# Kernel optimization log

Measured on AMD Instinct MI355X. Metric: run time of the kernel, lower is better.

Reference implementation:

```python
import jax, jax.numpy as jnp
import numpy as np

G = 128            # fine grid side -> N0 = 16384 nodes
C = 128            # hidden channels
CL = 4             # voxel cluster side (scale = CL/G = 1/32)
GC = G // CL       # coarse grid side = 32
NC = GC * GC       # 1024 coarse nodes
L = 6              # 3 MP blocks (down0, down1, up0) x 2 MP layers each


def _build_graph():
    ii, jj = np.meshgrid(np.arange(G), np.arange(G), indexing='ij')
    nid = ii * G + jj
    s_h, t_h = nid[:, :-1].ravel(), nid[:, 1:].ravel()
    s_v, t_v = nid[:-1, :].ravel(), nid[1:, :].ravel()
    src = np.concatenate([s_h, t_h, s_v, t_v]).astype(np.int64)
    dst = np.concatenate([t_h, s_h, t_v, s_v]).astype(np.int64)
    # voxel_grid(pos, size=1/32) on the unit square -> cluster id per node
    perm = ((ii // CL) * GC + (jj // CL)).ravel().astype(np.int64)
    ms, mt = perm[src], perm[dst]
    key = ms * NC + mt
    nonself = ms != mt
    uk = np.unique(key[nonself])                  # pool_edge: remove self loops + coalesce (sorted)
    E1 = int(uk.shape[0])
    e2c = np.where(nonself, np.searchsorted(uk, key), E1).astype(np.int64)
    pooled_ei = np.stack([uk // NC, uk % NC]).astype(np.int64)
    # unpool_edge: first fine edge whose mapped endpoints match each coarse edge
    first = np.full(E1 + 1, src.shape[0], dtype=np.int64)
    np.minimum.at(first, e2c, np.arange(src.shape[0], dtype=np.int64))
    perm_edges = first[:E1]
    return np.stack([src, dst]), perm, pooled_ei, e2c, perm_edges


def setup_inputs() -> dict:
    key = jax.random.key(0)
    ks = jax.random.split(key, 10)
    ei, perm, pei, e2c, pe = _build_graph()
    N0, E0 = G * G, ei.shape[1]
    s = 0.05
    return {
        'x': jax.random.normal(ks[0], (N0, C), jnp.float32),
        'edge_attr': jax.random.normal(ks[1], (E0, C), jnp.float32),
        'We1': jax.random.normal(ks[2], (L, 3 * C, C), jnp.float32) * s,
        'be1': jax.random.normal(ks[3], (L, C), jnp.float32) * s,
        'We2': jax.random.normal(ks[4], (L, C, C), jnp.float32) * s,
        'be2': jax.random.normal(ks[5], (L, C), jnp.float32) * s,
        'Wn1': jax.random.normal(ks[6], (L, 2 * C, C), jnp.float32) * s,
        'bn1': jax.random.normal(ks[7], (L, C), jnp.float32) * s,
        'Wn2': jax.random.normal(ks[8], (L, C, C), jnp.float32) * s,
        'bn2': jax.random.normal(ks[9], (L, C), jnp.float32) * s,
        'edge_index': jnp.asarray(ei),
        'perm': jnp.asarray(perm),
        'pooled_edge_index': jnp.asarray(pei),
        'edge_to_coarse': jnp.asarray(e2c),
        'perm_edges': jnp.asarray(pe),
    }


def _mp_block(x, e, src, dst, n, layers, We1, be1, We2, be2, Wn1, bn1, Wn2, bn2):
    # Residual message-passing block: edge MLP on [e, x_src, x_dst], node MLP on [x, sum_msg]
    for l in layers:
        m = jnp.concatenate([e, x[src], x[dst]], axis=-1)          # [E, 3C]
        e = e + (jax.nn.relu(m @ We1[l] + be1[l]) @ We2[l] + be2[l])
        agg = jax.ops.segment_sum(e, dst, num_segments=n)          # [N, C]
        h = jnp.concatenate([x, agg], axis=-1)                     # [N, 2C]
        x = x + (jax.nn.relu(h @ Wn1[l] + bn1[l]) @ Wn2[l] + bn2[l])
    return x, e


def reference(x, edge_attr, We1, be1, We2, be2, Wn1, bn1, Wn2, bn2,
              edge_index, perm, pooled_edge_index, edge_to_coarse, perm_edges):
    p = (We1, be1, We2, be2, Wn1, bn1, Wn2, bn2)
    N0 = x.shape[0]
    src0, dst0 = edge_index[0], edge_index[1]
    # down conv 0 (fine level)
    x0, e0 = _mp_block(x, edge_attr, src0, dst0, N0, (0, 1), *p)
    # avg_pool: mean node features per cluster, coalesce-sum edge attrs
    counts = jax.ops.segment_sum(jnp.ones((N0, 1), x.dtype), perm, num_segments=NC)
    x1 = jax.ops.segment_sum(x0, perm, num_segments=NC) / counts
    E1 = pooled_edge_index.shape[1]
    ea1 = jax.ops.segment_sum(e0, edge_to_coarse, num_segments=E1 + 1)[:E1]
    # down conv 1 (coarse level)
    x1, ea1 = _mp_block(x1, ea1, pooled_edge_index[0], pooled_edge_index[1], NC, (2, 3), *p)
    # unpool + sum-res skip connections
    xu = x0 + x1[perm]
    eu = e0 + jnp.zeros_like(e0).at[perm_edges].set(ea1)
    # up conv
    return _mp_block(xu, eu, src0, dst0, N0, (4, 5), *p)
```

## Files before the change

kernel.cpp:

```cpp
#include <hip/hip_runtime.h>

#define C_ 128
#define N0 16384
#define E0 65024
#define NC_ 1024
#define E1C 3968
#define LSTR 40

typedef __attribute__((ext_vector_type(8))) short bf16x8;
typedef __attribute__((ext_vector_type(4))) float f32x4;

#define OFF_WE1 0
#define OFF_WE2 294912
#define OFF_WN1 393216
#define OFF_WN2 589824
#define W_TOTAL 688128

__device__ __forceinline__ void bsplit(float a, unsigned short& hi, unsigned short& lo) {
  unsigned ab = __float_as_uint(a);
  unsigned hb = ab & 0xFFFF0000u;
  hi = (unsigned short)(hb >> 16);
  float r = a - __uint_as_float(hb);
  lo = (unsigned short)(__float_as_uint(r) >> 16);
}

__device__ __forceinline__ int cprefix(int ci, int cj) {
  int rows = (ci == 0) ? 0 : (94 + (ci - 1) * 126);
  int v = (ci > 0) + (ci < 31);
  int within = (cj == 0) ? 0 : (2 * cj - 1);
  return rows + within + cj * v;
}

__device__ __forceinline__ void add4(float4& s, const float* p) {
  float4 v = *(const float4*)p;
  s.x += v.x; s.y += v.y; s.z += v.z; s.w += v.w;
}

__global__ void prep_weights(const float* __restrict__ We1, const float* __restrict__ We2,
                             const float* __restrict__ Wn1, const float* __restrict__ Wn2,
                             short* __restrict__ wh, short* __restrict__ wl) {
  int idx = blockIdx.x * 256 + threadIdx.x;
  const float* src; int Kt, off, rem;
  if (idx < 294912)      { src = We1; Kt = 384; off = OFF_WE1; rem = idx; }
  else if (idx < 393216) { src = We2; Kt = 128; off = OFF_WE2; rem = idx - 294912; }
  else if (idx < 589824) { src = Wn1; Kt = 256; off = OFF_WN1; rem = idx - 393216; }
  else                   { src = Wn2; Kt = 128; off = OFF_WN2; rem = idx - 589824; }
  int per_layer = Kt << 7;
  int layer = rem / per_layer;
  int r2 = rem - layer * per_layer;
  int k = r2 >> 7;
  int col = r2 & 127;
  float a = src[layer * per_layer + (k << 7) + col];
  unsigned short hi, lo;
  bsplit(a, hi, lo);
  int dst = off + layer * ((Kt >> 5) << 12) + ((k >> 5) << 12) + (col << 5) + (k & 31);
  wh[dst] = (short)hi;
  wl[dst] = (short)lo;
}

template<int MODE>
__global__ __launch_bounds__(256, 2) void mlp_mfma(
    float* __restrict__ io, const float* __restrict__ xin,
    const int* __restrict__ srcI, const int* __restrict__ dstI,
    const short* __restrict__ W1h, const short* __restrict__ W1l,
    const float* __restrict__ b1,
    const short* __restrict__ W2h, const short* __restrict__ W2l,
    const float* __restrict__ b2)
{
  __shared__ alignas(16) short sAh[64 * LSTR], sAl[64 * LSTR];
  __shared__ alignas(16) short sWh[128 * LSTR], sWl[128 * LSTR];
  __shared__ int sS[64], sD[64];

  const int tid = threadIdx.x;
  const int r0 = blockIdx.x * 64;
  const int w   = tid >> 6;
  const int l   = tid & 63;
  const int c15 = l & 15;
  const int kg  = l >> 4;

  if (MODE == 0) {
    if (tid < 64) sS[tid] = srcI[r0 + tid];
    else if (tid < 128) sD[tid - 64] = dstI[r0 + tid - 64];
    __syncthreads();
  }

  f32x4 acc[8];
  #pragma unroll
  for (int t = 0; t < 8; ++t) acc[t] = (f32x4){0.f, 0.f, 0.f, 0.f};

  const int NKT = (MODE == 0) ? 12 : 8;
  for (int kt = 0; kt < NKT; ++kt) {
    const int region = kt >> 2;
    const int colbase = (kt & 3) * 32;
    #pragma unroll
    for (int tt = 0; tt < 2; ++tt) {
      int s = tid * 2 + tt;
      int row = s >> 3, q = s & 7;
      const float* rp;
      if (MODE == 0) {
        rp = (region == 0) ? io + (r0 + row) * C_
           : (region == 1) ? xin + sS[row] * C_
                           : xin + sD[row] * C_;
      } else {
        rp = (region == 0) ? io + (r0 + row) * C_ : xin + (r0 + row) * C_;
      }
      float4 a = *(const float4*)(rp + colbase + q * 4);
      unsigned short h0,h1,h2,h3, q0,q1,q2,q3;
      bsplit(a.x, h0, q0); bsplit(a.y, h1, q1);
      bsplit(a.z, h2, q2); bsplit(a.w, h3, q3);
      *(uint2*)&sAh[row * LSTR + q * 4] =
          make_uint2((unsigned)h0 | ((unsigned)h1 << 16), (unsigned)h2 | ((unsigned)h3 << 16));
      *(uint2*)&sAl[row * LSTR + q * 4] =
          make_uint2((unsigned)q0 | ((unsigned)q1 << 16), (unsigned)q2 | ((unsigned)q3 << 16));
    }
    {
      const short* srcH = W1h + (kt << 12);
      const short* srcL = W1l + (kt << 12);
      #pragma unroll
      for (int u0 = 0; u0 < 2; ++u0) {
        int u = tid + u0 * 256;
        int col = u >> 2, part = u & 3;
        *(uint4*)&sWh[col * LSTR + part * 8] = *(const uint4*)(srcH + u * 8);
        *(uint4*)&sWl[col * LSTR + part * 8] = *(const uint4*)(srcL + u * 8);
      }
    }
    __syncthreads();
    bf16x8 ah = *(const bf16x8*)&sAh[(w * 16 + c15) * LSTR + kg * 8];
    bf16x8 al = *(const bf16x8*)&sAl[(w * 16 + c15) * LSTR + kg * 8];
    #pragma unroll
    for (int t = 0; t < 8; ++t) {
      bf16x8 wh = *(const bf16x8*)&sWh[(t * 16 + c15) * LSTR + kg * 8];
      bf16x8 wl = *(const bf16x8*)&sWl[(t * 16 + c15) * LSTR + kg * 8];
      acc[t] = __builtin_amdgcn_mfma_f32_16x16x32_bf16(ah, wh, acc[t], 0, 0, 0);
      acc[t] = __builtin_amdgcn_mfma_f32_16x16x32_bf16(ah, wl, acc[t], 0, 0, 0);
      acc[t] = __builtin_amdgcn_mfma_f32_16x16x32_bf16(al, wh, acc[t], 0, 0, 0);
    }
    __syncthreads();
  }

  float b1v[8];
  #pragma unroll
  for (int t = 0; t < 8; ++t) b1v[t] = b1[t * 16 + c15];

  f32x4 acc2[8];
  #pragma unroll
  for (int t = 0; t < 8; ++t) acc2[t] = (f32x4){0.f, 0.f, 0.f, 0.f};

  #pragma unroll
  for (int kc = 0; kc < 4; ++kc) {
    __syncthreads();
    #pragma unroll
    for (int tt = 0; tt < 2; ++tt) {
      const int t = kc * 2 + tt;
      #pragma unroll
      for (int r = 0; r < 4; ++r) {
        float h = fmaxf(acc[t][r] + b1v[t], 0.f);
        unsigned short hh, hl;
        bsplit(h, hh, hl);
        int row = w * 16 + kg * 4 + r;
        int k = tt * 16 + c15;
        sAh[row * LSTR + k] = (short)hh;
        sAl[row * LSTR + k] = (short)hl;
      }
    }
    {
      const short* srcH = W2h + (kc << 12);
      const short* srcL = W2l + (kc << 12);
      #pragma unroll
      for (int u0 = 0; u0 < 2; ++u0) {
        int u = tid + u0 * 256;
        int col = u >> 2, part = u & 3;
        *(uint4*)&sWh[col * LSTR + part * 8] = *(const uint4*)(srcH + u * 8);
        *(uint4*)&sWl[col * LSTR + part * 8] = *(const uint4*)(srcL + u * 8);
      }
    }
    __syncthreads();
    bf16x8 ah = *(const bf16x8*)&sAh[(w * 16 + c15) * LSTR + kg * 8];
    bf16x8 al = *(const bf16x8*)&sAl[(w * 16 + c15) * LSTR + kg * 8];
    #pragma unroll
    for (int t = 0; t < 8; ++t) {
      bf16x8 wh = *(const bf16x8*)&sWh[(t * 16 + c15) * LSTR + kg * 8];
      bf16x8 wl = *(const bf16x8*)&sWl[(t * 16 + c15) * LSTR + kg * 8];
      acc2[t] = __builtin_amdgcn_mfma_f32_16x16x32_bf16(ah, wh, acc2[t], 0, 0, 0);
      acc2[t] = __builtin_amdgcn_mfma_f32_16x16x32_bf16(ah, wl, acc2[t], 0, 0, 0);
      acc2[t] = __builtin_amdgcn_mfma_f32_16x16x32_bf16(al, wh, acc2[t], 0, 0, 0);
    }
  }

  #pragma unroll
  for (int t = 0; t < 8; ++t) {
    float b2v = b2[t * 16 + c15];
    #pragma unroll
    for (int r = 0; r < 4; ++r) {
      int row = r0 + w * 16 + kg * 4 + r;
      float* p = io + row * C_ + t * 16 + c15;
      *p += acc2[t][r] + b2v;
    }
  }
}

__global__ void agg_fine(const float* __restrict__ e, float* __restrict__ agg) {
  int idx = blockIdx.x * 256 + threadIdx.x;
  int n = idx >> 5;
  int c4 = (idx & 31) * 4;
  int i = n >> 7, j = n & 127;
  float4 s = make_float4(0.f, 0.f, 0.f, 0.f);
  if (j >= 1)   add4(s, e + (i*127 + (j-1)) * C_ + c4);
  if (j <= 126) add4(s, e + (16256 + i*127 + j) * C_ + c4);
  if (i >= 1)   add4(s, e + (32512 + (i-1)*128 + j) * C_ + c4);
  if (i <= 126) add4(s, e + (48768 + i*128 + j) * C_ + c4);
  *(float4*)(agg + n * C_ + c4) = s;
}

__global__ void agg_coarse(const float* __restrict__ e1, float* __restrict__ agg1) {
  int idx = blockIdx.x * 256 + threadIdx.x;
  int m = idx >> 5;
  int c4 = (idx & 31) * 4;
  int ci = m >> 5, cj = m & 31;
  float4 s = make_float4(0.f, 0.f, 0.f, 0.f);
  if (ci > 0)  add4(s, e1 + (cprefix(ci-1,cj) + (ci-1>0) + (cj>0) + (cj<31)) * C_ + c4);
  if (cj > 0)  add4(s, e1 + (cprefix(ci,cj-1) + (ci>0) + (cj-1>0)) * C_ + c4);
  if (cj < 31) add4(s, e1 + (cprefix(ci,cj+1) + (ci>0)) * C_ + c4);
  if (ci < 31) add4(s, e1 + (cprefix(ci+1,cj)) * C_ + c4);
  *(float4*)(agg1 + m * C_ + c4) = s;
}

__global__ void pool_x(const float* __restrict__ x, float* __restrict__ x1) {
  int idx = blockIdx.x * 256 + threadIdx.x;
  int m = idx >> 5;
  int c4 = (idx & 31) * 4;
  int ci = m >> 5, cj = m & 31;
  float4 s = make_float4(0.f, 0.f, 0.f, 0.f);
  #pragma unroll
  for (int a = 0; a < 4; ++a)
    #pragma unroll
    for (int b = 0; b < 4; ++b)
      add4(s, x + ((4*ci + a) * 128 + 4*cj + b) * C_ + c4);
  s.x *= 0.0625f; s.y *= 0.0625f; s.z *= 0.0625f; s.w *= 0.0625f;
  *(float4*)(x1 + m * C_ + c4) = s;
}

__global__ void pool_e(const float* __restrict__ e, float* __restrict__ e1) {
  int idx = blockIdx.x * 256 + threadIdx.x;
  int combo = idx >> 5;
  int c4 = (idx & 31) * 4;
  int m = combo >> 2, dir = combo & 3;
  int ci = m >> 5, cj = m & 31;
  int cid, f0, fstep;
  if (dir == 0) { if (ci == 0) return;
    cid = cprefix(ci,cj);
    f0 = 48768 + (4*ci - 1) * 128 + 4*cj; fstep = 1;
  } else if (dir == 1) { if (cj == 0) return;
    cid = cprefix(ci,cj) + (ci>0);
    f0 = 16256 + (4*ci) * 127 + 4*cj - 1; fstep = 127;
  } else if (dir == 2) { if (cj == 31) return;
    cid = cprefix(ci,cj) + (ci>0) + (cj>0);
    f0 = (4*ci) * 127 + 4*cj + 3; fstep = 127;
  } else { if (ci == 31) return;
    cid = cprefix(ci,cj) + (ci>0) + (cj>0) + (cj<31);
    f0 = 32512 + (4*ci + 3) * 128 + 4*cj; fstep = 1;
  }
  float4 s = make_float4(0.f, 0.f, 0.f, 0.f);
  #pragma unroll
  for (int k = 0; k < 4; ++k)
    add4(s, e + (f0 + k * fstep) * C_ + c4);
  *(float4*)(e1 + cid * C_ + c4) = s;
}

__global__ void unpool_x(float* __restrict__ x, const float* __restrict__ x1,
                         const int* __restrict__ perm) {
  int idx = blockIdx.x * 256 + threadIdx.x;
  int n = idx >> 5, c4 = (idx & 31) * 4;
  int m = perm[n];
  float4 v = *(const float4*)(x + n * C_ + c4);
  add4(v, x1 + m * C_ + c4);
  *(float4*)(x + n * C_ + c4) = v;
}

__global__ void unpool_e(float* __restrict__ e, const float* __restrict__ e1,
                         const int* __restrict__ pe) {
  int idx = blockIdx.x * 256 + threadIdx.x;
  int k = idx >> 5, c4 = (idx & 31) * 4;
  int fe = pe[k];
  float4 v = *(const float4*)(e + fe * C_ + c4);
  add4(v, e1 + k * C_ + c4);
  *(float4*)(e + fe * C_ + c4) = v;
}

extern "C" void kernel_launch(void* const* d_in, const int* in_sizes, int n_in,
                              void* d_out, int out_size, void* d_ws, size_t ws_size,
                              hipStream_t stream) {
  const float* in_x  = (const float*)d_in[0];
  const float* in_ea = (const float*)d_in[1];
  const float* We1 = (const float*)d_in[2];
  const float* be1 = (const float*)d_in[3];
  const float* We2 = (const float*)d_in[4];
  const float* be2 = (const float*)d_in[5];
  const float* Wn1 = (const float*)d_in[6];
  const float* bn1 = (const float*)d_in[7];
  const float* Wn2 = (const float*)d_in[8];
  const float* bn2 = (const float*)d_in[9];
  const int* ei   = (const int*)d_in[10];
  const int* perm = (const int*)d_in[11];
  const int* pei  = (const int*)d_in[12];
  const int* pe   = (const int*)d_in[14];

  float* x = (float*)d_out;
  float* e = x + (size_t)N0 * C_;
  float* agg  = (float*)d_ws;
  float* x1   = agg + (size_t)N0 * C_;
  float* e1   = x1 + (size_t)NC_ * C_;
  float* agg1 = e1 + (size_t)E1C * C_;
  short* wsH  = (short*)(agg1 + (size_t)NC_ * C_);
  short* wsL  = wsH + W_TOTAL;

  hipMemcpyAsync(x, in_x, (size_t)N0 * C_ * 4, hipMemcpyDeviceToDevice, stream);
  hipMemcpyAsync(e, in_ea, (size_t)E0 * C_ * 4, hipMemcpyDeviceToDevice, stream);

  prep_weights<<<W_TOTAL / 256, 256, 0, stream>>>(We1, We2, Wn1, Wn2, wsH, wsL);

  const int* srcF = ei;  const int* dstF = ei + E0;
  const int* srcC = pei; const int* dstC = pei + E1C;

  #define WE1_OFF(l) (OFF_WE1 + (l) * 49152)
  #define WE2_OFF(l) (OFF_WE2 + (l) * 16384)
  #define WN1_OFF(l) (OFF_WN1 + (l) * 32768)
  #define WN2_OFF(l) (OFF_WN2 + (l) * 16384)

  for (int l = 0; l < 2; ++l) {
    mlp_mfma<0><<<E0/64, 256, 0, stream>>>(e, x, srcF, dstF,
        wsH + WE1_OFF(l), wsL + WE1_OFF(l), be1 + l*C_,
        wsH + WE2_OFF(l), wsL + WE2_OFF(l), be2 + l*C_);
    agg_fine<<<N0*32/256, 256, 0, stream>>>(e, agg);
    mlp_mfma<1><<<N0/64, 256, 0, stream>>>(x, agg, nullptr, nullptr,
        wsH + WN1_OFF(l), wsL + WN1_OFF(l), bn1 + l*C_,
        wsH + WN2_OFF(l), wsL + WN2_OFF(l), bn2 + l*C_);
  }

  pool_x<<<NC_*32/256, 256, 0, stream>>>(x, x1);
  pool_e<<<NC_*4*32/256, 256, 0, stream>>>(e, e1);

  for (int l = 2; l < 4; ++l) {
    mlp_mfma<0><<<E1C/64, 256, 0, stream>>>(e1, x1, srcC, dstC,
        wsH + WE1_OFF(l), wsL + WE1_OFF(l), be1 + l*C_,
        wsH + WE2_OFF(l), wsL + WE2_OFF(l), be2 + l*C_);
    agg_coarse<<<NC_*32/256, 256, 0, stream>>>(e1, agg1);
    mlp_mfma<1><<<NC_/64, 256, 0, stream>>>(x1, agg1, nullptr, nullptr,
        wsH + WN1_OFF(l), wsL + WN1_OFF(l), bn1 + l*C_,
        wsH + WN2_OFF(l), wsL + WN2_OFF(l), bn2 + l*C_);
  }

  unpool_x<<<N0*32/256, 256, 0, stream>>>(x, x1, perm);
  unpool_e<<<E1C*32/256, 256, 0, stream>>>(e, e1, pe);

  for (int l = 4; l < 6; ++l) {
    mlp_mfma<0><<<E0/64, 256, 0, stream>>>(e, x, srcF, dstF,
        wsH + WE1_OFF(l), wsL + WE1_OFF(l), be1 + l*C_,
        wsH + WE2_OFF(l), wsL + WE2_OFF(l), be2 + l*C_);
    agg_fine<<<N0*32/256, 256, 0, stream>>>(e, agg);
    mlp_mfma<1><<<N0/64, 256, 0, stream>>>(x, agg, nullptr, nullptr,
        wsH + WN1_OFF(l), wsL + WN1_OFF(l), bn1 + l*C_,
        wsH + WN2_OFF(l), wsL + WN2_OFF(l), bn2 + l*C_);
  }
}
```

Before: 475.3 us.

## Retile MLP kernel to 128-row blocks with 32x32 MFMA and register-prefetched A

Each block of the fused two-layer MLP kernel now covers 128 rows instead of 64. Its four waves are arranged 2x2, and each wave computes a 64x64 output tile with 32x32x16 bf16 MFMAs. A-operand rows are loaded straight from global memory into registers, split into hi/lo bf16 there, and the next k-chunk is prefetched before the barrier. The old LDS A staging buffer is gone, and the hidden activation is stored as packed hi/lo in a single LDS buffer. The aim is to halve weight staging per row, raise MFMA efficiency and cut LDS traffic, at the cost of higher register pressure and far fewer blocks (only 128 for node MLPs and 8 at the coarse level), which may leave many CUs idle.

```diff
diff --git a/kernel.cpp b/kernel.cpp
--- a/kernel.cpp
+++ b/kernel.cpp
@@ -6,9 +6,10 @@
 #define NC_ 1024
 #define E1C 3968
 #define LSTR 40
+#define HSTR 36
 
 typedef __attribute__((ext_vector_type(8))) short bf16x8;
-typedef __attribute__((ext_vector_type(4))) float f32x4;
+typedef __attribute__((ext_vector_type(16))) float f32x16;
 
 #define OFF_WE1 0
 #define OFF_WE2 294912
@@ -34,6 +35,13 @@
 __device__ __forceinline__ void add4(float4& s, const float* p) {
   float4 v = *(const float4*)p;
   s.x += v.x; s.y += v.y; s.z += v.z; s.w += v.w;
+}
+
+__device__ __forceinline__ f32x16 zero16() {
+  f32x16 z;
+  #pragma unroll
+  for (int i = 0; i < 16; ++i) z[i] = 0.f;
+  return z;
 }
 
 __global__ void prep_weights(const float* __restrict__ We1, const float* __restrict__ We2,
@@ -58,6 +66,44 @@
   wl[dst] = (short)lo;
 }
 
+__device__ __forceinline__ void stage_w(short* sWh, short* sWl,
+                                        const short* __restrict__ Wh,
+                                        const short* __restrict__ Wl,
+                                        int kc, int tid) {
+  const short* srcH = Wh + (kc << 12);
+  const short* srcL = Wl + (kc << 12);
+  #pragma unroll
+  for (int u0 = 0; u0 < 2; ++u0) {
+    int u = tid + u0 * 256;
+    int col = u >> 2, part = u & 3;
+    *(uint4*)&sWh[col * LSTR + part * 8] = *(const uint4*)(srcH + u * 8);
+    *(uint4*)&sWl[col * LSTR + part * 8] = *(const uint4*)(srcL + u * 8);
+  }
+}
+
+#define BSPLIT8(V0, V1, AH, AL) do { \
+    unsigned short h0_,h1_,h2_,h3_,h4_,h5_,h6_,h7_, l0_,l1_,l2_,l3_,l4_,l5_,l6_,l7_; \
+    bsplit((V0).x,h0_,l0_); bsplit((V0).y,h1_,l1_); bsplit((V0).z,h2_,l2_); bsplit((V0).w,h3_,l3_); \
+    bsplit((V1).x,h4_,l4_); bsplit((V1).y,h5_,l5_); bsplit((V1).z,h6_,l6_); bsplit((V1).w,h7_,l7_); \
+    AH = (bf16x8){(short)h0_,(short)h1_,(short)h2_,(short)h3_,(short)h4_,(short)h5_,(short)h6_,(short)h7_}; \
+    AL = (bf16x8){(short)l0_,(short)l1_,(short)l2_,(short)l3_,(short)l4_,(short)l5_,(short)l6_,(short)l7_}; \
+  } while (0)
+
+#define MFMA3(ACC, AH, AL, BH, BL) do { \
+    ACC = __builtin_amdgcn_mfma_f32_32x32x16_bf16(AH, BH, ACC, 0, 0, 0); \
+    ACC = __builtin_amdgcn_mfma_f32_32x32x16_bf16(AH, BL, ACC, 0, 0, 0); \
+    ACC = __builtin_amdgcn_mfma_f32_32x32x16_bf16(AL, BH, ACC, 0, 0, 0); \
+  } while (0)
+
+#define UNPACKH(ROW, S, AH, AL) do { \
+    const unsigned* hp_ = &sH[(ROW) * HSTR + (S) * 16 + hi * 8]; \
+    uint4 u0_ = *(const uint4*)hp_; uint4 u1_ = *(const uint4*)(hp_ + 4); \
+    AH = (bf16x8){(short)(u0_.x & 0xFFFFu), (short)(u0_.y & 0xFFFFu), (short)(u0_.z & 0xFFFFu), (short)(u0_.w & 0xFFFFu), \
+                  (short)(u1_.x & 0xFFFFu), (short)(u1_.y & 0xFFFFu), (short)(u1_.z & 0xFFFFu), (short)(u1_.w & 0xFFFFu)}; \
+    AL = (bf16x8){(short)(u0_.x >> 16), (short)(u0_.y >> 16), (short)(u0_.z >> 16), (short)(u0_.w >> 16), \
+                  (short)(u1_.x >> 16), (short)(u1_.y >> 16), (short)(u1_.z >> 16), (short)(u1_.w >> 16)}; \
+  } while (0)
+
 template<int MODE>
 __global__ __launch_bounds__(256, 2) void mlp_mfma(
     float* __restrict__ io, const float* __restrict__ xin,
@@ -67,136 +113,133 @@
     const short* __restrict__ W2h, const short* __restrict__ W2l,
     const float* __restrict__ b2)
 {
-  __shared__ alignas(16) short sAh[64 * LSTR], sAl[64 * LSTR];
   __shared__ alignas(16) short sWh[128 * LSTR], sWl[128 * LSTR];
-  __shared__ int sS[64], sD[64];
+  __shared__ alignas(16) unsigned sH[128 * HSTR];
 
   const int tid = threadIdx.x;
-  const int r0 = blockIdx.x * 64;
   const int w   = tid >> 6;
+  const int wr  = w >> 1;
+  const int wc  = w & 1;
   const int l   = tid & 63;
-  const int c15 = l & 15;
-  const int kg  = l >> 4;
-
+  const int c31 = l & 31;
+  const int hi  = l >> 5;
+  const int r0  = blockIdx.x * 128;
+
+  const int ar0 = wr * 64 + c31;
+  const int ar1 = ar0 + 32;
+  const float* pio0 = io + (size_t)(r0 + ar0) * C_;
+  const float* pio1 = io + (size_t)(r0 + ar1) * C_;
+  const float *px0, *px1, *pd0, *pd1;
   if (MODE == 0) {
-    if (tid < 64) sS[tid] = srcI[r0 + tid];
-    else if (tid < 128) sD[tid - 64] = dstI[r0 + tid - 64];
+    px0 = xin + (size_t)srcI[r0 + ar0] * C_;
+    px1 = xin + (size_t)srcI[r0 + ar1] * C_;
+    pd0 = xin + (size_t)dstI[r0 + ar0] * C_;
+    pd1 = xin + (size_t)dstI[r0 + ar1] * C_;
+  } else {
+    px0 = xin + (size_t)(r0 + ar0) * C_;
+    px1 = xin + (size_t)(r0 + ar1) * C_;
+    pd0 = px0; pd1 = px1;
+  }
+
+  float4 pa00, pa01, pa02, pa03, pa10, pa11, pa12, pa13;
+#define LOADA(KC) do { \
+    int rg_ = (KC) >> 2; int cb_ = ((KC) & 3) * 32 + hi * 8; \
+    const float* q0_; const float* q1_; \
+    if (MODE == 0) { q0_ = (rg_ == 0) ? pio0 : (rg_ == 1) ? px0 : pd0; \
+                     q1_ = (rg_ == 0) ? pio1 : (rg_ == 1) ? px1 : pd1; } \
+    else           { q0_ = (rg_ == 0) ? pio0 : px0; \
+                     q1_ = (rg_ == 0) ? pio1 : px1; } \
+    pa00 = *(const float4*)(q0_ + cb_);      pa01 = *(const float4*)(q0_ + cb_ + 4); \
+    pa02 = *(const float4*)(q0_ + cb_ + 16); pa03 = *(const float4*)(q0_ + cb_ + 20); \
+    pa10 = *(const float4*)(q1_ + cb_);      pa11 = *(const float4*)(q1_ + cb_ + 4); \
+    pa12 = *(const float4*)(q1_ + cb_ + 16); pa13 = *(const float4*)(q1_ + cb_ + 20); \
+  } while (0)
+
+  f32x16 acc00 = zero16(), acc01 = zero16(), acc10 = zero16(), acc11 = zero16();
+
+  const int NK1 = (MODE == 0) ? 12 : 8;
+  LOADA(0);
+  for (int kc = 0; kc < NK1; ++kc) {
+    bf16x8 ah0s0, al0s0, ah0s1, al0s1, ah1s0, al1s0, ah1s1, al1s1;
+    BSPLIT8(pa00, pa01, ah0s0, al0s0);
+    BSPLIT8(pa02, pa03, ah0s1, al0s1);
+    BSPLIT8(pa10, pa11, ah1s0, al1s0);
+    BSPLIT8(pa12, pa13, ah1s1, al1s1);
+    if (kc + 1 < NK1) LOADA(kc + 1);
     __syncthreads();
-  }
-
-  f32x4 acc[8];
-  #pragma unroll
-  for (int t = 0; t < 8; ++t) acc[t] = (f32x4){0.f, 0.f, 0.f, 0.f};
-
-  const int NKT = (MODE == 0) ? 12 : 8;
-  for (int kt = 0; kt < NKT; ++kt) {
-    const int region = kt >> 2;
-    const int colbase = (kt & 3) * 32;
+    stage_w(sWh, sWl, W1h, W1l, kc, tid);
+    __syncthreads();
     #pragma unroll
-    for (int tt = 0; tt < 2; ++tt) {
-      int s = tid * 2 + tt;
-      int row = s >> 3, q = s & 7;
-      const float* rp;
-      if (MODE == 0) {
-        rp = (region == 0) ? io + (r0 + row) * C_
-           : (region == 1) ? xin + sS[row] * C_
-                           : xin + sD[row] * C_;
+    for (int s = 0; s < 2; ++s) {
+      const int wb = s * 16 + hi * 8;
+      bf16x8 bh0 = *(const bf16x8*)&sWh[(wc * 64 + c31) * LSTR + wb];
+      bf16x8 bl0 = *(const bf16x8*)&sWl[(wc * 64 + c31) * LSTR + wb];
+      bf16x8 bh1 = *(const bf16x8*)&sWh[(wc * 64 + 32 + c31) * LSTR + wb];
+      bf16x8 bl1 = *(const bf16x8*)&sWl[(wc * 64 + 32 + c31) * LSTR + wb];
+      if (s == 0) {
+        MFMA3(acc00, ah0s0, al0s0, bh0, bl0);
+        MFMA3(acc01, ah0s0, al0s0, bh1, bl1);
+        MFMA3(acc10, ah1s0, al1s0, bh0, bl0);
+        MFMA3(acc11, ah1s0, al1s0, bh1, bl1);
       } else {
-        rp = (region == 0) ? io + (r0 + row) * C_ : xin + (r0 + row) * C_;
-      }
-      float4 a = *(const float4*)(rp + colbase + q * 4);
-      unsigned short h0,h1,h2,h3, q0,q1,q2,q3;
-      bsplit(a.x, h0, q0); bsplit(a.y, h1, q1);
-      bsplit(a.z, h2, q2); bsplit(a.w, h3, q3);
-      *(uint2*)&sAh[row * LSTR + q * 4] =
-          make_uint2((unsigned)h0 | ((unsigned)h1 << 16), (unsigned)h2 | ((unsigned)h3 << 16));
-      *(uint2*)&sAl[row * LSTR + q * 4] =
-          make_uint2((unsigned)q0 | ((unsigned)q1 << 16), (unsigned)q2 | ((unsigned)q3 << 16));
-    }
-    {
-      const short* srcH = W1h + (kt << 12);
-      const short* srcL = W1l + (kt << 12);
-      #pragma unroll
-      for (int u0 = 0; u0 < 2; ++u0) {
-        int u = tid + u0 * 256;
-        int col = u >> 2, part = u & 3;
-        *(uint4*)&sWh[col * LSTR + part * 8] = *(const uint4*)(srcH + u * 8);
-        *(uint4*)&sWl[col * LSTR + part * 8] = *(const uint4*)(srcL + u * 8);
+        MFMA3(acc00, ah0s1, al0s1, bh0, bl0);
+        MFMA3(acc01, ah0s1, al0s1, bh1, bl1);
+        MFMA3(acc10, ah1s1, al1s1, bh0, bl0);
+        MFMA3(acc11, ah1s1, al1s1, bh1, bl1);
       }
     }
-    __syncthreads();
-    bf16x8 ah = *(const bf16x8*)&sAh[(w * 16 + c15) * LSTR + kg * 8];
-    bf16x8 al = *(const bf16x8*)&sAl[(w * 16 + c15) * LSTR + kg * 8];
-    #pragma unroll
-    for (int t = 0; t < 8; ++t) {
-      bf16x8 wh = *(const bf16x8*)&sWh[(t * 16 + c15) * LSTR + kg * 8];
-      bf16x8 wl = *(const bf16x8*)&sWl[(t * 16 + c15) * LSTR + kg * 8];
-      acc[t] = __builtin_amdgcn_mfma_f32_16x16x32_bf16(ah, wh, acc[t], 0, 0, 0);
-      acc[t] = __builtin_amdgcn_mfma_f32_16x16x32_bf16(ah, wl, acc[t], 0, 0, 0);
-      acc[t] = __builtin_amdgcn_mfma_f32_16x16x32_bf16(al, wh, acc[t], 0, 0, 0);
-    }
-    __syncthreads();
-  }
-
-  float b1v[8];
-  #pragma unroll
-  for (int t = 0; t < 8; ++t) b1v[t] = b1[t * 16 + c15];
-
-  f32x4 acc2[8];
-  #pragma unroll
-  for (int t = 0; t < 8; ++t) acc2[t] = (f32x4){0.f, 0.f, 0.f, 0.f};
-
+  }
+
+  f32x16 bcc00 = zero16(), bcc01 = zero16(), bcc10 = zero16(), bcc11 = zero16();
   #pragma unroll
   for (int kc = 0; kc < 4; ++kc) {
     __syncthreads();
-    #pragma unroll
-    for (int tt = 0; tt < 2; ++tt) {
-      const int t = kc * 2 + tt;
+    if (wc == (kc >> 1)) {
+      const float bb = b1[(kc >> 1) * 64 + (kc & 1) * 32 + c31];
       #pragma unroll
-      for (int r = 0; r < 4; ++r) {
-        float h = fmaxf(acc[t][r] + b1v[t], 0.f);
+      for (int rg = 0; rg < 16; ++rg) {
+        int rr = (rg & 3) + 8 * (rg >> 2) + 4 * hi;
+        float h0 = fmaxf(((kc & 1) ? acc01[rg] : acc00[rg]) + bb, 0.f);
+        float h1 = fmaxf(((kc & 1) ? acc11[rg] : acc10[rg]) + bb, 0.f);
         unsigned short hh, hl;
-        bsplit(h, hh, hl);
-        int row = w * 16 + kg * 4 + r;
-        int k = tt * 16 + c15;
-        sAh[row * LSTR + k] = (short)hh;
-        sAl[row * LSTR + k] = (short)hl;
+        bsplit(h0, hh, hl);
+        sH[(wr * 64 + rr) * HSTR + c31] = (unsigned)hh | ((unsigned)hl << 16);
+        bsplit(h1, hh, hl);
+        sH[(wr * 64 + 32 + rr) * HSTR + c31] = (unsigned)hh | ((unsigned)hl << 16);
       }
     }
-    {
-      const short* srcH = W2h + (kc << 12);
-      const short* srcL = W2l + (kc << 12);
-      #pragma unroll
-      for (int u0 = 0; u0 < 2; ++u0) {
-        int u = tid + u0 * 256;
-        int col = u >> 2, part = u & 3;
-        *(uint4*)&sWh[col * LSTR + part * 8] = *(const uint4*)(srcH + u * 8);
-        *(uint4*)&sWl[col * LSTR + part * 8] = *(const uint4*)(srcL + u * 8);
-      }
+    stage_w(sWh, sWl, W2h, W2l, kc, tid);
+    __syncthreads();
+    #pragma unroll
+    for (int s = 0; s < 2; ++s) {
+      bf16x8 ah0, al0, ah1, al1;
+      UNPACKH(wr * 64 + c31, s, ah0, al0);
+      UNPACKH(wr * 64 + 32 + c31, s, ah1, al1);
+      const int wb = s * 16 + hi * 8;
+      bf16x8 bh0 = *(const bf16x8*)&sWh[(wc * 64 + c31) * LSTR + wb];
+      bf16x8 bl0 = *(const bf16x8*)&sWl[(wc * 64 + c31) * LSTR + wb];
+      bf16x8 bh1 = *(const bf16x8*)&sWh[(wc * 64 + 32 + c31) * LSTR + wb];
+      bf16x8 bl1 = *(const bf16x8*)&sWl[(wc * 64 + 32 + c31) * LSTR + wb];
+      MFMA3(bcc00, ah0, al0, bh0, bl0);
+      MFMA3(bcc01, ah0, al0, bh1, bl1);
+      MFMA3(bcc10, ah1, al1, bh0, bl0);
+      MFMA3(bcc11, ah1, al1, bh1, bl1);
     }
-    __syncthreads();
-    bf16x8 ah = *(const bf16x8*)&sAh[(w * 16 + c15) * LSTR + kg * 8];
-    bf16x8 al = *(const bf16x8*)&sAl[(w * 16 + c15) * LSTR + kg * 8];
-    #pragma unroll
-    for (int t = 0; t < 8; ++t) {
-      bf16x8 wh = *(const bf16x8*)&sWh[(t * 16 + c15) * LSTR + kg * 8];
-      bf16x8 wl = *(const bf16x8*)&sWl[(t * 16 + c15) * LSTR + kg * 8];
-      acc2[t] = __builtin_amdgcn_mfma_f32_16x16x32_bf16(ah, wh, acc2[t], 0, 0, 0);
-      acc2[t] = __builtin_amdgcn_mfma_f32_16x16x32_bf16(ah, wl, acc2[t], 0, 0, 0);
-      acc2[t] = __builtin_amdgcn_mfma_f32_16x16x32_bf16(al, wh, acc2[t], 0, 0, 0);
-    }
-  }
-
-  #pragma unroll
-  for (int t = 0; t < 8; ++t) {
-    float b2v = b2[t * 16 + c15];
-    #pragma unroll
-    for (int r = 0; r < 4; ++r) {
-      int row = r0 + w * 16 + kg * 4 + r;
-      float* p = io + row * C_ + t * 16 + c15;
-      *p += acc2[t][r] + b2v;
-    }
-  }
+  }
+
+  const float b2c0 = b2[wc * 64 + c31];
+  const float b2c1 = b2[wc * 64 + 32 + c31];
+  #pragma unroll
+  for (int rg = 0; rg < 16; ++rg) {
+    int rr = (rg & 3) + 8 * (rg >> 2) + 4 * hi;
+    size_t row0 = (size_t)(r0 + wr * 64 + rr) * C_;
+    size_t row1 = (size_t)(r0 + wr * 64 + 32 + rr) * C_;
+    io[row0 + wc * 64 + c31]      += bcc00[rg] + b2c0;
+    io[row0 + wc * 64 + 32 + c31] += bcc01[rg] + b2c1;
+    io[row1 + wc * 64 + c31]      += bcc10[rg] + b2c0;
+    io[row1 + wc * 64 + 32 + c31] += bcc11[rg] + b2c1;
+  }
+#undef LOADA
 }
 
 __global__ void agg_fine(const float* __restrict__ e, float* __restrict__ agg) {
@@ -328,11 +371,11 @@
   #define WN2_OFF(l) (OFF_WN2 + (l) * 16384)
 
   for (int l = 0; l < 2; ++l) {
-    mlp_mfma<0><<<E0/64, 256, 0, stream>>>(e, x, srcF, dstF,
+    mlp_mfma<0><<<E0/128, 256, 0, stream>>>(e, x, srcF, dstF,
         wsH + WE1_OFF(l), wsL + WE1_OFF(l), be1 + l*C_,
         wsH + WE2_OFF(l), wsL + WE2_OFF(l), be2 + l*C_);
     agg_fine<<<N0*32/256, 256, 0, stream>>>(e, agg);
-    mlp_mfma<1><<<N0/64, 256, 0, stream>>>(x, agg, nullptr, nullptr,
+    mlp_mfma<1><<<N0/128, 256, 0, stream>>>(x, agg, nullptr, nullptr,
         wsH + WN1_OFF(l), wsL + WN1_OFF(l), bn1 + l*C_,
         wsH + WN2_OFF(l), wsL + WN2_OFF(l), bn2 + l*C_);
   }
@@ -341,11 +384,11 @@
   pool_e<<<NC_*4*32/256, 256, 0, stream>>>(e, e1);
 
   for (int l = 2; l < 4; ++l) {
-    mlp_mfma<0><<<E1C/64, 256, 0, stream>>>(e1, x1, srcC, dstC,
+    mlp_mfma<0><<<E1C/128, 256, 0, stream>>>(e1, x1, srcC, dstC,
         wsH + WE1_OFF(l), wsL + WE1_OFF(l), be1 + l*C_,
         wsH + WE2_OFF(l), wsL + WE2_OFF(l), be2 + l*C_);
     agg_coarse<<<NC_*32/256, 256, 0, stream>>>(e1, agg1);
-    mlp_mfma<1><<<NC_/64, 256, 0, stream>>>(x1, agg1, nullptr, nullptr,
+    mlp_mfma<1><<<NC_/128, 256, 0, stream>>>(x1, agg1, nullptr, nullptr,
         wsH + WN1_OFF(l), wsL + WN1_OFF(l), bn1 + l*C_,
         wsH + WN2_OFF(l), wsL + WN2_OFF(l), bn2 + l*C_);
   }
@@ -354,11 +397,11 @@
   unpool_e<<<E1C*32/256, 256, 0, stream>>>(e, e1, pe);
 
   for (int l = 4; l < 6; ++l) {
-    mlp_mfma<0><<<E0/64, 256, 0, stream>>>(e, x, srcF, dstF,
+    mlp_mfma<0><<<E0/128, 256, 0, stream>>>(e, x, srcF, dstF,
         wsH + WE1_OFF(l), wsL + WE1_OFF(l), be1 + l*C_,
         wsH + WE2_OFF(l), wsL + WE2_OFF(l), be2 + l*C_);
     agg_fine<<<N0*32/256, 256, 0, stream>>>(e, agg);
-    mlp_mfma<1><<<N0/64, 256, 0, stream>>>(x, agg, nullptr, nullptr,
+    mlp_mfma<1><<<N0/128, 256, 0, stream>>>(x, agg, nullptr, nullptr,
         wsH + WN1_OFF(l), wsL + WN1_OFF(l), bn1 + l*C_,
         wsH + WN2_OFF(l), wsL + WN2_OFF(l), bn2 + l*C_);
   }
```

New measurement: 548.7 us. 1.15x slower.
